# Performance work log

Measured on AMD Instinct MI355X. Metric: run time of the kernel, lower is better.

The kernel has to match this reference:

```python
import jax, jax.numpy as jnp
import numpy as np
import math

LMAX = 3
_EPS = 1e-7


def _np_J(ell):
    """Precompute J^l = diag((-1)^i) @ d^l(pi/2) in float64 numpy (constant)."""
    if ell == 0:
        return np.ones((1, 1))
    c = math.cos(math.pi / 4.0)
    s = math.sin(math.pi / 4.0)
    fact = [1.0]
    for i in range(1, 2 * ell + 2):
        fact.append(fact[-1] * i)
    dim = 2 * ell + 1
    d = np.zeros((dim, dim))
    for mi in range(dim):
        m = ell - mi
        for mpi in range(dim):
            mp = ell - mpi
            pref = math.sqrt(fact[ell + m] * fact[ell - m] * fact[ell + mp] * fact[ell - mp])
            val = 0.0
            for k in range(max(0, m - mp), min(ell + m, ell - mp) + 1):
                denom = fact[ell + m - k] * fact[ell - mp - k] * fact[k + mp - m] * fact[k]
                val += ((-1) ** (m - mp + k)) * pref / denom * c ** (2 * ell + mp - m - 2 * k) * s ** (m - mp + 2 * k)
            d[mi, mpi] = val
    signs = np.array([(-1) ** i for i in range(dim)])
    return signs[:, None] * d


_J_MATS = [_np_J(ell) for ell in range(LMAX + 1)]


def _z_rot(angle, ell):
    """Real-SH z-rotation matrix [E, 2l+1, 2l+1]; m ordered l..-l.
    Z[i, rev(i)] = sin(m_i*phi), Z[i, i] = cos(m_i*phi) (diag set last so m=0 cell = cos(0)=1)."""
    dim = 2 * ell + 1
    m = jnp.arange(ell, -ell - 1, -1, dtype=angle.dtype)  # [dim]
    idx = np.arange(dim)
    rev = idx[::-1].copy()
    Z = jnp.zeros((angle.shape[0], dim, dim), dtype=angle.dtype)
    ph = angle[:, None] * m  # [E, dim]
    Z = Z.at[:, idx, rev].set(jnp.sin(ph))
    Z = Z.at[:, idx, idx].set(jnp.cos(ph))
    return Z


def reference(edge_vec):
    """Per-edge block-diagonal Wigner D (ZYZ, D^l = Z(a) J Z(b) J Z(g)).
    edge_vec: [E, 3] -> [E, (LMAX+1)^2, (LMAX+1)^2]."""
    dtype = edge_vec.dtype
    x, y, z = edge_vec[:, 0], edge_vec[:, 1], edge_vec[:, 2]
    r = jnp.sqrt(jnp.sum(edge_vec * edge_vec, axis=-1))
    cos_beta = jnp.clip(z / jnp.maximum(r, _EPS), -1.0 + _EPS, 1.0 - _EPS)  # safe acos
    beta = jnp.arccos(cos_beta)
    degenerate = (jnp.abs(x) < _EPS) & (jnp.abs(y) < _EPS)  # safe atan2
    x_safe = jnp.where(degenerate, jnp.ones_like(x), x)
    alpha = jnp.where(degenerate, jnp.zeros_like(x), jnp.arctan2(y, x_safe))
    gamma = jnp.zeros_like(alpha)

    E = edge_vec.shape[0]
    full_dim = (LMAX + 1) ** 2
    out = jnp.zeros((E, full_dim, full_dim), dtype=dtype)
    off = 0
    for ell in range(LMAX + 1):
        dim = 2 * ell + 1
        J = jnp.asarray(_J_MATS[ell], dtype=dtype)  # [dim, dim]
        Za = _z_rot(alpha, ell)
        Zb = _z_rot(beta, ell)
        Zg = _z_rot(gamma, ell)
        Dl = Za @ J @ Zb @ J @ Zg  # [E, dim, dim]
        out = out.at[:, off:off + dim, off:off + dim].set(Dl)
        off += dim
    return out


def setup_inputs() -> dict:
    key = jax.random.key(0)
    edge_vec = jax.random.normal(key, (400000, 3), dtype=jnp.float32)
    return {"edge_vec": edge_vec}
```

## Files before the change

kernel.cpp:

```cpp
#include <hip/hip_runtime.h>
#include <math.h>

constexpr double csqrt(double a) {
    double x = a > 1.0 ? a : 1.0;
    for (int i = 0; i < 48; ++i) x = 0.5 * (x + a / x);
    return x;
}

constexpr double j_entry_d(int ell, int mi, int mpi) {
    if (ell == 0) return 1.0;
    double fact[8] = {1.0, 1.0, 2.0, 6.0, 24.0, 120.0, 720.0, 5040.0};
    int m  = ell - mi;
    int mp = ell - mpi;
    double pref  = csqrt(fact[ell + m] * fact[ell - m] * fact[ell + mp] * fact[ell - mp]);
    double scale = 1.0 / (double)(1 << ell);
    int k0 = (m - mp) > 0 ? (m - mp) : 0;
    int k1 = (ell + m) < (ell - mp) ? (ell + m) : (ell - mp);
    double val = 0.0;
    for (int k = k0; k <= k1; ++k) {
        double denom = fact[ell + m - k] * fact[ell - mp - k] * fact[k + mp - m] * fact[k];
        double t = pref / denom * scale;
        val += ((m - mp + k) & 1) ? -t : t;
    }
    return (mi & 1) ? -val : val;
}

struct alignas(16) Tabs { float t[64][48]; };

constexpr Tabs make_tabs() {
    Tabs T{};
    for (int lane = 0; lane < 64; ++lane) {
        int r = lane >> 2, c = lane & 3;
        int L  = (r == 0) ? 0 : (r < 4) ? 1 : (r < 9) ? 2 : 3;
        int li = r - L * L;
        int m_i = L - li;
        int am  = m_i < 0 ? -m_i : m_i;
        for (int s = 0; s < 7; ++s) {
            int ms  = 3 - s;
            int ams = ms < 0 ? -ms : ms;
            bool in = (ams <= L);
            int  kp = L - ms;
            T.t[lane][s]     = in ? (float)j_entry_d(L, li, kp) : 0.0f;
            T.t[lane][7 + s] = in ? (float)j_entry_d(L, 2 * L - li, kp) : 0.0f;
            for (int j = 0; j < 4; ++j) {
                int v = 4 * c + j - L * L;
                T.t[lane][14 + 4 * s + j] =
                    (in && v >= 0 && v <= 2 * L) ? (float)j_entry_d(L, kp, v) : 0.0f;
            }
        }
        T.t[lane][42] = (float)am;
        T.t[lane][43] = (m_i < 0) ? -1.0f : 1.0f;
        T.t[lane][44] = 0.0f; T.t[lane][45] = 0.0f;
        T.t[lane][46] = 0.0f; T.t[lane][47] = 0.0f;
    }
    return T;
}

__device__ constexpr Tabs g_tabs = make_tabs();

__global__ __launch_bounds__(256)
void EdgeRotation_49435073577214_kernel(const float* __restrict__ ev,
                                        float* __restrict__ out,
                                        int E, int nwaves) {
    const int lane = (int)(threadIdx.x & 63);
    int wv = (int)(blockIdx.x * (blockDim.x >> 6) + (threadIdx.x >> 6));
    wv = __builtin_amdgcn_readfirstlane(wv);

    const float* tp = g_tabs.t[lane];
    float jmu[7], jrev[7], M[7][4];
#pragma unroll
    for (int s = 0; s < 7; ++s) { jmu[s] = tp[s]; jrev[s] = tp[7 + s]; }
#pragma unroll
    for (int s = 0; s < 7; ++s)
#pragma unroll
        for (int j = 0; j < 4; ++j) M[s][j] = tp[14 + 4 * s + j];
    const float amf = tp[42], sgn = tp[43];

    int e  = wv;
    int ep = e < E ? e : 0;
    float x = ev[3 * ep], y = ev[3 * ep + 1], z = ev[3 * ep + 2];

    while (e < E) {
        const int en  = e + nwaves;
        const int epn = en < E ? en : 0;
        const float xn = ev[3 * epn], yn = ev[3 * epn + 1], zn = ev[3 * epn + 2];

        const float r2   = fmaf(x, x, fmaf(y, y, z * z));
        const float rho2 = fmaf(x, x, y * y);
        const float rinv = __builtin_amdgcn_rsqf(fmaxf(r2, 1e-30f));
        float cb = z * rinv;
        cb = fminf(fmaxf(cb, -1.0f + 1e-7f), 1.0f - 1e-7f);
        const float sb = __builtin_amdgcn_sqrtf(fmaxf(fmaf(-cb, cb, 1.0f), 0.0f));

        const float rhoinv = __builtin_amdgcn_rsqf(fmaxf(rho2, 1e-30f));
        const bool  nd  = rho2 >= 1e-14f;
        const float ca1 = nd ? x * rhoinv : 1.0f;
        const float sa1 = nd ? y * rhoinv : 0.0f;

        const float CA2 = fmaf(ca1, ca1, -(sa1 * sa1));
        const float SA2 = 2.0f * ca1 * sa1;
        const float CA3 = fmaf(CA2, ca1, -(SA2 * sa1));
        const float SA3 = fmaf(SA2, ca1, CA2 * sa1);
        const float CB2 = fmaf(cb, cb, -(sb * sb));
        const float SB2 = 2.0f * cb * sb;
        const float CB3 = fmaf(CB2, cb, -(SB2 * sb));
        const float SB3 = fmaf(SB2, cb, CB2 * sb);

        float ca = amf == 0.0f ? 1.0f : amf == 1.0f ? ca1 : amf == 2.0f ? CA2 : CA3;
        float sa = amf == 0.0f ? 0.0f : amf == 1.0f ? sa1 : amf == 2.0f ? SA2 : SA3;
        sa *= sgn;

        float u[7];
#pragma unroll
        for (int s = 0; s < 7; ++s) u[s] = fmaf(ca, jmu[s], sa * jrev[s]);

        float w[7];
        w[0] = fmaf(-u[6], SB3, u[0] * CB3);
        w[1] = fmaf(-u[5], SB2, u[1] * CB2);
        w[2] = fmaf(-u[4], sb , u[2] * cb );
        w[3] = u[3];
        w[4] = fmaf( u[2], sb , u[4] * cb );
        w[5] = fmaf( u[1], SB2, u[5] * CB2);
        w[6] = fmaf( u[0], SB3, u[6] * CB3);

        float a0 = 0.f, a1 = 0.f, a2 = 0.f, a3 = 0.f;
#pragma unroll
        for (int s = 0; s < 7; ++s) {
            a0 = fmaf(w[s], M[s][0], a0);
            a1 = fmaf(w[s], M[s][1], a1);
            a2 = fmaf(w[s], M[s][2], a2);
            a3 = fmaf(w[s], M[s][3], a3);
        }

        reinterpret_cast<float4*>(out + ((size_t)e << 8))[lane] =
            make_float4(a0, a1, a2, a3);

        x = xn; y = yn; z = zn; e = en;
    }
}

extern "C" void kernel_launch(void* const* d_in, const int* in_sizes, int n_in,
                              void* d_out, int out_size, void* d_ws, size_t ws_size,
                              hipStream_t stream) {
    const float* ev  = (const float*)d_in[0];
    float*       out = (float*)d_out;
    int E = in_sizes[0] / 3;

    dim3 grid(2048), block(256);
    int nwaves = (int)((2048 * 256) / 64);
    hipLaunchKernelGGL(EdgeRotation_49435073577214_kernel, grid, block, 0, stream,
                       ev, out, E, nwaves);
}
```

Baseline: 101.5 us.

## Unroll edge loop by four, use nontemporal stores, and make order selection branchless

Each wave now processes four edges per loop iteration, issuing all twelve coordinate loads up front instead of prefetching one edge ahead. Output writes become nontemporal vector stores so the 400 MB output stream bypasses cache retention. The per-lane angular-order select chain is replaced by one-hot FMA weights from the constant table, with the sign folded into the table. This aims to improve memory-level parallelism and store throughput on a write-bound kernel, at the cost of more registers and some redundant clamped work at the tail.

```diff
diff --git a/kernel.cpp b/kernel.cpp
--- a/kernel.cpp
+++ b/kernel.cpp
@@ -1,5 +1,7 @@
 #include <hip/hip_runtime.h>
 #include <math.h>
+
+typedef float vfloat4 __attribute__((ext_vector_type(4)));
 
 constexpr double csqrt(double a) {
     double x = a > 1.0 ? a : 1.0;
@@ -35,28 +37,90 @@
         int li = r - L * L;
         int m_i = L - li;
         int am  = m_i < 0 ? -m_i : m_i;
+        double sgn = (m_i < 0) ? -1.0 : 1.0;
         for (int s = 0; s < 7; ++s) {
             int ms  = 3 - s;
             int ams = ms < 0 ? -ms : ms;
             bool in = (ams <= L);
             int  kp = L - ms;
             T.t[lane][s]     = in ? (float)j_entry_d(L, li, kp) : 0.0f;
-            T.t[lane][7 + s] = in ? (float)j_entry_d(L, 2 * L - li, kp) : 0.0f;
+            T.t[lane][7 + s] = in ? (float)(sgn * j_entry_d(L, 2 * L - li, kp)) : 0.0f;
             for (int j = 0; j < 4; ++j) {
                 int v = 4 * c + j - L * L;
                 T.t[lane][14 + 4 * s + j] =
                     (in && v >= 0 && v <= 2 * L) ? (float)j_entry_d(L, kp, v) : 0.0f;
             }
         }
-        T.t[lane][42] = (float)am;
-        T.t[lane][43] = (m_i < 0) ? -1.0f : 1.0f;
-        T.t[lane][44] = 0.0f; T.t[lane][45] = 0.0f;
+        T.t[lane][42] = (am == 0) ? 1.0f : 0.0f;
+        T.t[lane][43] = (am == 1) ? 1.0f : 0.0f;
+        T.t[lane][44] = (am == 2) ? 1.0f : 0.0f;
+        T.t[lane][45] = (am == 3) ? 1.0f : 0.0f;
         T.t[lane][46] = 0.0f; T.t[lane][47] = 0.0f;
     }
     return T;
 }
 
 __device__ constexpr Tabs g_tabs = make_tabs();
+
+struct LaneCst {
+    float jmu[7], jrv[7], M[7][4];
+    float sA0, sA1, sA2, sA3;
+};
+
+__device__ __forceinline__ vfloat4 edge_mat(float x, float y, float z, const LaneCst& C) {
+    const float xx   = x * x;
+    const float r2   = fmaf(z, z, fmaf(y, y, xx));
+    const float rho2 = fmaf(y, y, xx);
+    const float rinv = __builtin_amdgcn_rsqf(fmaxf(r2, 1e-30f));
+    float cb = z * rinv;
+    cb = fminf(fmaxf(cb, -1.0f + 1e-7f), 1.0f - 1e-7f);
+    const float sb = __builtin_amdgcn_sqrtf(fmaxf(fmaf(-cb, cb, 1.0f), 0.0f));
+
+    const float rhoinv = __builtin_amdgcn_rsqf(fmaxf(rho2, 1e-30f));
+    const bool  nd  = rho2 >= 1e-14f;
+    const float ca1 = nd ? x * rhoinv : 1.0f;
+    const float sa1 = nd ? y * rhoinv : 0.0f;
+
+    const float CA2 = fmaf(ca1, ca1, -(sa1 * sa1));
+    const float SA2 = 2.0f * ca1 * sa1;
+    const float CA3 = fmaf(CA2, ca1, -(SA2 * sa1));
+    const float SA3 = fmaf(SA2, ca1, CA2 * sa1);
+    const float CB2 = fmaf(cb, cb, -(sb * sb));
+    const float SB2 = 2.0f * cb * sb;
+    const float CB3 = fmaf(CB2, cb, -(SB2 * sb));
+    const float SB3 = fmaf(SB2, cb, CB2 * sb);
+
+    float ca = fmaf(C.sA1, ca1, C.sA0);
+    ca = fmaf(C.sA2, CA2, ca);
+    ca = fmaf(C.sA3, CA3, ca);
+    float sa = C.sA1 * sa1;
+    sa = fmaf(C.sA2, SA2, sa);
+    sa = fmaf(C.sA3, SA3, sa);
+
+    float u[7];
+#pragma unroll
+    for (int s = 0; s < 7; ++s) u[s] = fmaf(ca, C.jmu[s], sa * C.jrv[s]);
+
+    float w[7];
+    w[0] = fmaf(-u[6], SB3, u[0] * CB3);
+    w[1] = fmaf(-u[5], SB2, u[1] * CB2);
+    w[2] = fmaf(-u[4], sb , u[2] * cb );
+    w[3] = u[3];
+    w[4] = fmaf( u[2], sb , u[4] * cb );
+    w[5] = fmaf( u[1], SB2, u[5] * CB2);
+    w[6] = fmaf( u[0], SB3, u[6] * CB3);
+
+    float a0 = 0.f, a1 = 0.f, a2 = 0.f, a3 = 0.f;
+#pragma unroll
+    for (int s = 0; s < 7; ++s) {
+        a0 = fmaf(w[s], C.M[s][0], a0);
+        a1 = fmaf(w[s], C.M[s][1], a1);
+        a2 = fmaf(w[s], C.M[s][2], a2);
+        a3 = fmaf(w[s], C.M[s][3], a3);
+    }
+    vfloat4 o; o.x = a0; o.y = a1; o.z = a2; o.w = a3;
+    return o;
+}
 
 __global__ __launch_bounds__(256)
 void EdgeRotation_49435073577214_kernel(const float* __restrict__ ev,
@@ -66,76 +130,48 @@
     int wv = (int)(blockIdx.x * (blockDim.x >> 6) + (threadIdx.x >> 6));
     wv = __builtin_amdgcn_readfirstlane(wv);
 
+    LaneCst C;
     const float* tp = g_tabs.t[lane];
-    float jmu[7], jrev[7], M[7][4];
 #pragma unroll
-    for (int s = 0; s < 7; ++s) { jmu[s] = tp[s]; jrev[s] = tp[7 + s]; }
+    for (int s = 0; s < 7; ++s) { C.jmu[s] = tp[s]; C.jrv[s] = tp[7 + s]; }
 #pragma unroll
     for (int s = 0; s < 7; ++s)
 #pragma unroll
-        for (int j = 0; j < 4; ++j) M[s][j] = tp[14 + 4 * s + j];
-    const float amf = tp[42], sgn = tp[43];
+        for (int j = 0; j < 4; ++j) C.M[s][j] = tp[14 + 4 * s + j];
+    C.sA0 = tp[42]; C.sA1 = tp[43]; C.sA2 = tp[44]; C.sA3 = tp[45];
 
-    int e  = wv;
-    int ep = e < E ? e : 0;
-    float x = ev[3 * ep], y = ev[3 * ep + 1], z = ev[3 * ep + 2];
+    const int Em1 = E - 1;
+    for (int e0 = wv; e0 < E; e0 += 4 * nwaves) {
+        const int e1 = e0 + nwaves;
+        const int e2 = e0 + 2 * nwaves;
+        const int e3 = e0 + 3 * nwaves;
+        const int c1 = e1 < E ? e1 : Em1;
+        const int c2 = e2 < E ? e2 : Em1;
+        const int c3 = e3 < E ? e3 : Em1;
 
-    while (e < E) {
-        const int en  = e + nwaves;
-        const int epn = en < E ? en : 0;
-        const float xn = ev[3 * epn], yn = ev[3 * epn + 1], zn = ev[3 * epn + 2];
+        const float x0 = ev[3 * e0], y0 = ev[3 * e0 + 1], z0 = ev[3 * e0 + 2];
+        const float x1 = ev[3 * c1], y1 = ev[3 * c1 + 1], z1 = ev[3 * c1 + 2];
+        const float x2 = ev[3 * c2], y2 = ev[3 * c2 + 1], z2 = ev[3 * c2 + 2];
+        const float x3 = ev[3 * c3], y3 = ev[3 * c3 + 1], z3 = ev[3 * c3 + 2];
 
-        const float r2   = fmaf(x, x, fmaf(y, y, z * z));
-        const float rho2 = fmaf(x, x, y * y);
-        const float rinv = __builtin_amdgcn_rsqf(fmaxf(r2, 1e-30f));
-        float cb = z * rinv;
-        cb = fminf(fmaxf(cb, -1.0f + 1e-7f), 1.0f - 1e-7f);
-        const float sb = __builtin_amdgcn_sqrtf(fmaxf(fmaf(-cb, cb, 1.0f), 0.0f));
+        const vfloat4 o0 = edge_mat(x0, y0, z0, C);
+        __builtin_nontemporal_store(o0,
+            reinterpret_cast<vfloat4*>(out + ((size_t)e0 << 8)) + lane);
 
-        const float rhoinv = __builtin_amdgcn_rsqf(fmaxf(rho2, 1e-30f));
-        const bool  nd  = rho2 >= 1e-14f;
-        const float ca1 = nd ? x * rhoinv : 1.0f;
-        const float sa1 = nd ? y * rhoinv : 0.0f;
+        const vfloat4 o1 = edge_mat(x1, y1, z1, C);
+        if (e1 < E)
+            __builtin_nontemporal_store(o1,
+                reinterpret_cast<vfloat4*>(out + ((size_t)e1 << 8)) + lane);
 
-        const float CA2 = fmaf(ca1, ca1, -(sa1 * sa1));
-        const float SA2 = 2.0f * ca1 * sa1;
-        const float CA3 = fmaf(CA2, ca1, -(SA2 * sa1));
-        const float SA3 = fmaf(SA2, ca1, CA2 * sa1);
-        const float CB2 = fmaf(cb, cb, -(sb * sb));
-        const float SB2 = 2.0f * cb * sb;
-        const float CB3 = fmaf(CB2, cb, -(SB2 * sb));
-        const float SB3 = fmaf(SB2, cb, CB2 * sb);
+        const vfloat4 o2 = edge_mat(x2, y2, z2, C);
+        if (e2 < E)
+            __builtin_nontemporal_store(o2,
+                reinterpret_cast<vfloat4*>(out + ((size_t)e2 << 8)) + lane);
 
-        float ca = amf == 0.0f ? 1.0f : amf == 1.0f ? ca1 : amf == 2.0f ? CA2 : CA3;
-        float sa = amf == 0.0f ? 0.0f : amf == 1.0f ? sa1 : amf == 2.0f ? SA2 : SA3;
-        sa *= sgn;
-
-        float u[7];
-#pragma unroll
-        for (int s = 0; s < 7; ++s) u[s] = fmaf(ca, jmu[s], sa * jrev[s]);
-
-        float w[7];
-        w[0] = fmaf(-u[6], SB3, u[0] * CB3);
-        w[1] = fmaf(-u[5], SB2, u[1] * CB2);
-        w[2] = fmaf(-u[4], sb , u[2] * cb );
-        w[3] = u[3];
-        w[4] = fmaf( u[2], sb , u[4] * cb );
-        w[5] = fmaf( u[1], SB2, u[5] * CB2);
-        w[6] = fmaf( u[0], SB3, u[6] * CB3);
-
-        float a0 = 0.f, a1 = 0.f, a2 = 0.f, a3 = 0.f;
-#pragma unroll
-        for (int s = 0; s < 7; ++s) {
-            a0 = fmaf(w[s], M[s][0], a0);
-            a1 = fmaf(w[s], M[s][1], a1);
-            a2 = fmaf(w[s], M[s][2], a2);
-            a3 = fmaf(w[s], M[s][3], a3);
-        }
-
-        reinterpret_cast<float4*>(out + ((size_t)e << 8))[lane] =
-            make_float4(a0, a1, a2, a3);
-
-        x = xn; y = yn; z = zn; e = en;
+        const vfloat4 o3 = edge_mat(x3, y3, z3, C);
+        if (e3 < E)
+            __builtin_nontemporal_store(o3,
+                reinterpret_cast<vfloat4*>(out + ((size_t)e3 << 8)) + lane);
     }
 }
 
```

After: 102.4 us. Within noise of the previous version (+0.9%).

## Compute one row per lane for four edges per wave and stage through LDS

Applied to the files above, without the earlier changes.

The kernel now maps 16 lanes to the 16 output rows of one edge, so each wave handles four edges at once. Each lane computes a full 7-column row with a 7x7 register matrix, scatters it into a zero-filled LDS tile, then reads it back as float4 and writes it with nontemporal stores. The angle selection becomes one-hot FMAs instead of compare chains, launch bounds ask for higher occupancy, and the next-edge prefetch is dropped. The aim is to cut redundant per-edge angle math and the store overhead per edge, at the cost of LDS traffic and more registers per lane.

```diff
diff --git a/kernel.cpp b/kernel.cpp
--- a/kernel.cpp
+++ b/kernel.cpp
@@ -1,5 +1,7 @@
 #include <hip/hip_runtime.h>
 #include <math.h>
+
+typedef float vfloat4 __attribute__((ext_vector_type(4)));
 
 constexpr double csqrt(double a) {
     double x = a > 1.0 ? a : 1.0;
@@ -25,117 +27,149 @@
     return (mi & 1) ? -val : val;
 }
 
-struct alignas(16) Tabs { float t[64][48]; };
+struct alignas(16) RowTabs { float t[16][68]; };
 
-constexpr Tabs make_tabs() {
-    Tabs T{};
-    for (int lane = 0; lane < 64; ++lane) {
-        int r = lane >> 2, c = lane & 3;
-        int L  = (r == 0) ? 0 : (r < 4) ? 1 : (r < 9) ? 2 : 3;
-        int li = r - L * L;
+constexpr RowTabs make_tabs() {
+    RowTabs T{};
+    for (int il = 0; il < 16; ++il) {
+        int L  = (il == 0) ? 0 : (il < 4) ? 1 : (il < 9) ? 2 : 3;
+        int li = il - L * L;
         int m_i = L - li;
         int am  = m_i < 0 ? -m_i : m_i;
+        double sgn = (m_i < 0) ? -1.0 : 1.0;
         for (int s = 0; s < 7; ++s) {
             int ms  = 3 - s;
             int ams = ms < 0 ? -ms : ms;
             bool in = (ams <= L);
             int  kp = L - ms;
-            T.t[lane][s]     = in ? (float)j_entry_d(L, li, kp) : 0.0f;
-            T.t[lane][7 + s] = in ? (float)j_entry_d(L, 2 * L - li, kp) : 0.0f;
-            for (int j = 0; j < 4; ++j) {
-                int v = 4 * c + j - L * L;
-                T.t[lane][14 + 4 * s + j] =
-                    (in && v >= 0 && v <= 2 * L) ? (float)j_entry_d(L, kp, v) : 0.0f;
-            }
+            T.t[il][s]     = in ? (float)j_entry_d(L, li, kp) : 0.0f;
+            T.t[il][7 + s] = in ? (float)(sgn * j_entry_d(L, 2 * L - li, kp)) : 0.0f;
+            for (int v = 0; v < 7; ++v)
+                T.t[il][14 + 7 * s + v] =
+                    (in && v <= 2 * L) ? (float)j_entry_d(L, kp, v) : 0.0f;
         }
-        T.t[lane][42] = (float)am;
-        T.t[lane][43] = (m_i < 0) ? -1.0f : 1.0f;
-        T.t[lane][44] = 0.0f; T.t[lane][45] = 0.0f;
-        T.t[lane][46] = 0.0f; T.t[lane][47] = 0.0f;
+        T.t[il][63] = (am == 0) ? 1.0f : 0.0f;
+        T.t[il][64] = (am == 1) ? 1.0f : 0.0f;
+        T.t[il][65] = (am == 2) ? 1.0f : 0.0f;
+        T.t[il][66] = (am == 3) ? 1.0f : 0.0f;
+        T.t[il][67] = 0.0f;
     }
     return T;
 }
 
-__device__ constexpr Tabs g_tabs = make_tabs();
+__device__ constexpr RowTabs g_tabs = make_tabs();
 
-__global__ __launch_bounds__(256)
+__global__ __launch_bounds__(256, 4)
 void EdgeRotation_49435073577214_kernel(const float* __restrict__ ev,
                                         float* __restrict__ out,
                                         int E, int nwaves) {
-    const int lane = (int)(threadIdx.x & 63);
-    int wv = (int)(blockIdx.x * (blockDim.x >> 6) + (threadIdx.x >> 6));
-    wv = __builtin_amdgcn_readfirstlane(wv);
+    __shared__ float lds[4][1024];
 
-    const float* tp = g_tabs.t[lane];
-    float jmu[7], jrev[7], M[7][4];
+    const int tid  = (int)threadIdx.x;
+    const int lane = tid & 63;
+    const int wib  = tid >> 6;
+    const int g    = lane >> 4;
+    const int il   = lane & 15;
+    float* wlds = lds[wib];
+
+    const int gw = (int)blockIdx.x * 4 + wib;
+
+    float jmu[7], jrv[7], M[7][7], sA0, sA1, sA2, sA3;
+    {
+        const float* tp = g_tabs.t[il];
 #pragma unroll
-    for (int s = 0; s < 7; ++s) { jmu[s] = tp[s]; jrev[s] = tp[7 + s]; }
+        for (int s = 0; s < 7; ++s) { jmu[s] = tp[s]; jrv[s] = tp[7 + s]; }
 #pragma unroll
-    for (int s = 0; s < 7; ++s)
+        for (int s = 0; s < 7; ++s)
 #pragma unroll
-        for (int j = 0; j < 4; ++j) M[s][j] = tp[14 + 4 * s + j];
-    const float amf = tp[42], sgn = tp[43];
+            for (int v = 0; v < 7; ++v) M[s][v] = tp[14 + 7 * s + v];
+        sA0 = tp[63]; sA1 = tp[64]; sA2 = tp[65]; sA3 = tp[66];
+    }
+    const int LL = (il == 0) ? 0 : (il < 4) ? 1 : (il < 9) ? 4 : 9;
+    float* pS = wlds + g * 256 + il * 16 + LL;
 
-    int e  = wv;
-    int ep = e < E ? e : 0;
-    float x = ev[3 * ep], y = ev[3 * ep + 1], z = ev[3 * ep + 2];
+    const int Em1 = E - 1;
+    for (int e0 = 4 * gw; e0 < E; e0 += 4 * nwaves) {
+        int eg = e0 + g;
+        eg = eg < E ? eg : Em1;
 
-    while (e < E) {
-        const int en  = e + nwaves;
-        const int epn = en < E ? en : 0;
-        const float xn = ev[3 * epn], yn = ev[3 * epn + 1], zn = ev[3 * epn + 2];
+        const float x = ev[3 * eg], y = ev[3 * eg + 1], z = ev[3 * eg + 2];
 
-        const float r2   = fmaf(x, x, fmaf(y, y, z * z));
-        const float rho2 = fmaf(x, x, y * y);
+        const float xx   = x * x;
+        const float r2   = fmaf(z, z, fmaf(y, y, xx));
+        const float rho2 = fmaf(y, y, xx);
         const float rinv = __builtin_amdgcn_rsqf(fmaxf(r2, 1e-30f));
-        float cb = z * rinv;
-        cb = fminf(fmaxf(cb, -1.0f + 1e-7f), 1.0f - 1e-7f);
-        const float sb = __builtin_amdgcn_sqrtf(fmaxf(fmaf(-cb, cb, 1.0f), 0.0f));
-
+        float cbv = z * rinv;
+        cbv = fminf(fmaxf(cbv, -1.0f + 1e-7f), 1.0f - 1e-7f);
+        const float sbv = __builtin_amdgcn_sqrtf(fmaxf(fmaf(-cbv, cbv, 1.0f), 0.0f));
         const float rhoinv = __builtin_amdgcn_rsqf(fmaxf(rho2, 1e-30f));
-        const bool  nd  = rho2 >= 1e-14f;
-        const float ca1 = nd ? x * rhoinv : 1.0f;
-        const float sa1 = nd ? y * rhoinv : 0.0f;
+        const bool  ndg = rho2 >= 1e-14f;
+        const float ca1 = ndg ? x * rhoinv : 1.0f;
+        const float sa1 = ndg ? y * rhoinv : 0.0f;
 
         const float CA2 = fmaf(ca1, ca1, -(sa1 * sa1));
         const float SA2 = 2.0f * ca1 * sa1;
         const float CA3 = fmaf(CA2, ca1, -(SA2 * sa1));
         const float SA3 = fmaf(SA2, ca1, CA2 * sa1);
-        const float CB2 = fmaf(cb, cb, -(sb * sb));
-        const float SB2 = 2.0f * cb * sb;
-        const float CB3 = fmaf(CB2, cb, -(SB2 * sb));
-        const float SB3 = fmaf(SB2, cb, CB2 * sb);
+        const float CB2 = fmaf(cbv, cbv, -(sbv * sbv));
+        const float SB2 = 2.0f * cbv * sbv;
+        const float CB3 = fmaf(CB2, cbv, -(SB2 * sbv));
+        const float SB3 = fmaf(SB2, cbv, CB2 * sbv);
 
-        float ca = amf == 0.0f ? 1.0f : amf == 1.0f ? ca1 : amf == 2.0f ? CA2 : CA3;
-        float sa = amf == 0.0f ? 0.0f : amf == 1.0f ? sa1 : amf == 2.0f ? SA2 : SA3;
-        sa *= sgn;
+        float ca = fmaf(sA1, ca1, sA0);
+        ca = fmaf(sA2, CA2, ca);
+        ca = fmaf(sA3, CA3, ca);
+        float sa = sA1 * sa1;
+        sa = fmaf(sA2, SA2, sa);
+        sa = fmaf(sA3, SA3, sa);
 
         float u[7];
 #pragma unroll
-        for (int s = 0; s < 7; ++s) u[s] = fmaf(ca, jmu[s], sa * jrev[s]);
+        for (int s = 0; s < 7; ++s) u[s] = fmaf(ca, jmu[s], sa * jrv[s]);
 
         float w[7];
         w[0] = fmaf(-u[6], SB3, u[0] * CB3);
         w[1] = fmaf(-u[5], SB2, u[1] * CB2);
-        w[2] = fmaf(-u[4], sb , u[2] * cb );
+        w[2] = fmaf(-u[4], sbv, u[2] * cbv);
         w[3] = u[3];
-        w[4] = fmaf( u[2], sb , u[4] * cb );
+        w[4] = fmaf( u[2], sbv, u[4] * cbv);
         w[5] = fmaf( u[1], SB2, u[5] * CB2);
         w[6] = fmaf( u[0], SB3, u[6] * CB3);
 
-        float a0 = 0.f, a1 = 0.f, a2 = 0.f, a3 = 0.f;
+        {
+            vfloat4 zz; zz.x = 0.f; zz.y = 0.f; zz.z = 0.f; zz.w = 0.f;
+            vfloat4* wv4 = reinterpret_cast<vfloat4*>(wlds);
+            wv4[lane]       = zz;
+            wv4[lane + 64]  = zz;
+            wv4[lane + 128] = zz;
+            wv4[lane + 192] = zz;
+        }
 #pragma unroll
-        for (int s = 0; s < 7; ++s) {
-            a0 = fmaf(w[s], M[s][0], a0);
-            a1 = fmaf(w[s], M[s][1], a1);
-            a2 = fmaf(w[s], M[s][2], a2);
-            a3 = fmaf(w[s], M[s][3], a3);
+        for (int v = 0; v < 7; ++v) {
+            float d = 0.f;
+#pragma unroll
+            for (int s = 0; s < 7; ++s) d = fmaf(w[s], M[s][v], d);
+            pS[v] = d;
         }
 
-        reinterpret_cast<float4*>(out + ((size_t)e << 8))[lane] =
-            make_float4(a0, a1, a2, a3);
-
-        x = xn; y = yn; z = zn; e = en;
+        const vfloat4* rv4 = reinterpret_cast<const vfloat4*>(wlds);
+        if (e0 + 4 <= E) {
+#pragma unroll
+            for (int q = 0; q < 4; ++q) {
+                vfloat4 o = rv4[q * 64 + lane];
+                __builtin_nontemporal_store(o,
+                    reinterpret_cast<vfloat4*>(out) + (size_t)(e0 + q) * 64 + lane);
+            }
+        } else {
+#pragma unroll
+            for (int q = 0; q < 4; ++q) {
+                if (e0 + q < E) {
+                    vfloat4 o = rv4[q * 64 + lane];
+                    __builtin_nontemporal_store(o,
+                        reinterpret_cast<vfloat4*>(out) + (size_t)(e0 + q) * 64 + lane);
+                }
+            }
+        }
     }
 }
 
```

Result: faster. 83.32 us (-17.9%).
